# Optimization experiments

Measured on AMD Instinct MI355X. Metric: run time of the kernel, lower is better.

## Reference

```python
import jax, jax.numpy as jnp
import numpy as np

N_LOC = 500000
N_CAT = 5000
N_EDGES = 2000000
LOC_DIM = 128
CAT_DIM = 128
INITRANGE = 0.1
NEG_SLOPE = 0.2


def setup_inputs() -> dict:
    key = jax.random.key(0)
    k1, k2, k3, k4 = jax.random.split(key, 4)
    loc_emb = jax.random.normal(k1, (N_LOC, LOC_DIM), dtype=jnp.float32)
    # loc_to_cat Linear params, init per init_weights(): uniform(-0.1, 0.1) weight, zero bias
    W = jax.random.uniform(k2, (CAT_DIM, LOC_DIM), dtype=jnp.float32,
                           minval=-INITRANGE, maxval=INITRANGE)
    b = jnp.zeros((CAT_DIM,), dtype=jnp.float32)
    edge_src = jax.random.randint(k3, (N_EDGES,), 0, N_LOC, dtype=jnp.int64)
    edge_dst = jax.random.randint(k4, (N_EDGES,), 0, N_CAT, dtype=jnp.int64)
    return {"loc_emb": loc_emb, "W": W, "b": b,
            "edge_src": edge_src, "edge_dst": edge_dst}


def reference(loc_emb, W, b, edge_src, edge_dst):
    # copy_u('f','m') + sum('m','in') across all canonical etypes, combined with 'sum':
    # gather source (loc) features along edges, segment-sum into cat nodes.
    msg = loc_emb[edge_src]                                   # [E, loc_dim]
    agg = jax.ops.segment_sum(msg, edge_dst, num_segments=N_CAT)  # [n_cat, loc_dim]
    # loc_to_cat linear + LeakyReLU(0.2)
    cat_emb = jax.nn.leaky_relu(agg @ W.T + b, negative_slope=NEG_SLOPE)
    return cat_emb
```

## Files before the change

### kernel.cpp

```cpp
#include <hip/hip_runtime.h>

#define N_LOC   500000
#define N_CAT   5000
#define N_EDGES 2000000
#define DIM     128
#define NEG_SLOPE 0.2f
#define PAD     5008
#define NB      128
#define EPB     15628

__launch_bounds__(1024)
__global__ void blockhist_kernel(const int* __restrict__ edst, const float* __restrict__ W,
                                 float* __restrict__ WT, int* __restrict__ rank,
                                 int* __restrict__ bhist) {
    int b = blockIdx.x, t = threadIdx.x;
    if (b == NB) {
        for (int i = t; i < DIM * DIM; i += 1024) {
            int j = i >> 7, k = i & 127;
            WT[k * DIM + j] = W[j * DIM + k];
        }
        return;
    }
    __shared__ int lh[N_CAT];
    for (int c = t; c < N_CAT; c += 1024) lh[c] = 0;
    __syncthreads();
    int s = b * EPB;
    int e = min(s + EPB, N_EDGES);
    int i = s + 4 * t;
    for (; i + 4 <= e; i += 4096) {
        int4 d = *(const int4*)(edst + i);
        int4 r;
        r.x = atomicAdd(&lh[d.x], 1);
        r.y = atomicAdd(&lh[d.y], 1);
        r.z = atomicAdd(&lh[d.z], 1);
        r.w = atomicAdd(&lh[d.w], 1);
        *(int4*)(rank + i) = r;
    }
    if (i < e) {
        int lim = min(i + 4, e);
        for (int j = i; j < lim; ++j) rank[j] = atomicAdd(&lh[edst[j]], 1);
    }
    __syncthreads();
    for (int c = t; c < N_CAT; c += 1024)
        bhist[(size_t)b * N_CAT + c] = lh[c];
}

__launch_bounds__(256)
__global__ void blockscan_kernel(int* __restrict__ bhist, int* __restrict__ tot) {
    int c = blockIdx.x * 256 + threadIdx.x;
    if (c >= N_CAT) return;
    int run = 0;
    for (int b0 = 0; b0 < NB; b0 += 8) {
        int v0 = bhist[(size_t)(b0 + 0) * N_CAT + c];
        int v1 = bhist[(size_t)(b0 + 1) * N_CAT + c];
        int v2 = bhist[(size_t)(b0 + 2) * N_CAT + c];
        int v3 = bhist[(size_t)(b0 + 3) * N_CAT + c];
        int v4 = bhist[(size_t)(b0 + 4) * N_CAT + c];
        int v5 = bhist[(size_t)(b0 + 5) * N_CAT + c];
        int v6 = bhist[(size_t)(b0 + 6) * N_CAT + c];
        int v7 = bhist[(size_t)(b0 + 7) * N_CAT + c];
        bhist[(size_t)(b0 + 0) * N_CAT + c] = run; run += v0;
        bhist[(size_t)(b0 + 1) * N_CAT + c] = run; run += v1;
        bhist[(size_t)(b0 + 2) * N_CAT + c] = run; run += v2;
        bhist[(size_t)(b0 + 3) * N_CAT + c] = run; run += v3;
        bhist[(size_t)(b0 + 4) * N_CAT + c] = run; run += v4;
        bhist[(size_t)(b0 + 5) * N_CAT + c] = run; run += v5;
        bhist[(size_t)(b0 + 6) * N_CAT + c] = run; run += v6;
        bhist[(size_t)(b0 + 7) * N_CAT + c] = run; run += v7;
    }
    tot[c] = run;
}

__launch_bounds__(1024)
__global__ void scan_kernel(const int* __restrict__ cnt, int* __restrict__ offsets) {
    __shared__ int wsum[16];
    __shared__ int woff[16];
    __shared__ int total_s, running_s;
    int t = threadIdx.x;
    int lane = t & 63, w = t >> 6;
    if (t == 0) { running_s = 0; offsets[0] = 0; }
    __syncthreads();
    for (int base = 0; base < N_CAT; base += 1024) {
        int i = base + t;
        int v = (i < N_CAT) ? cnt[i] : 0;
        int incl = v;
        #pragma unroll
        for (int off = 1; off < 64; off <<= 1) {
            int x = __shfl_up(incl, off, 64);
            if (lane >= off) incl += x;
        }
        if (lane == 63) wsum[w] = incl;
        __syncthreads();
        if (w == 0 && lane < 16) {
            int s = wsum[lane];
            int e = s;
            #pragma unroll
            for (int off = 1; off < 16; off <<= 1) {
                int x = __shfl_up(e, off, 64);
                if (lane >= off) e += x;
            }
            woff[lane] = e - s;
            if (lane == 15) total_s = e;
        }
        __syncthreads();
        int run = running_s;
        if (i < N_CAT) offsets[i + 1] = run + woff[w] + incl;
        __syncthreads();
        if (t == 0) running_s = run + total_s;
        __syncthreads();
    }
}

__global__ void fill2_kernel(const int* __restrict__ esrc, const int* __restrict__ edst,
                             const int* __restrict__ rank, const int* __restrict__ offsets,
                             const int* __restrict__ bhist, int* __restrict__ csr_src) {
    int i4 = (blockIdx.x * blockDim.x + threadIdx.x) * 4;
    if (i4 + 4 <= N_EDGES) {
        int4 c = *(const int4*)(edst + i4);
        int4 s = *(const int4*)(esrc + i4);
        int4 r = *(const int4*)(rank + i4);
        size_t bb = (size_t)(i4 / EPB) * N_CAT;
        csr_src[offsets[c.x] + bhist[bb + c.x] + r.x] = s.x;
        csr_src[offsets[c.y] + bhist[bb + c.y] + r.y] = s.y;
        csr_src[offsets[c.z] + bhist[bb + c.z] + r.z] = s.z;
        csr_src[offsets[c.w] + bhist[bb + c.w] + r.w] = s.w;
    } else {
        for (int i = i4; i < N_EDGES; ++i) {
            int c = edst[i];
            size_t bb = (size_t)(i / EPB) * N_CAT;
            csr_src[offsets[c] + bhist[bb + c] + rank[i]] = esrc[i];
        }
    }
}

__launch_bounds__(256)
__global__ void agg_fused_kernel(const float* __restrict__ loc, const int* __restrict__ csr_src,
                                 const int* __restrict__ offsets, const float* __restrict__ WT,
                                 const float* __restrict__ bias, float* __restrict__ out) {
    __shared__ float4 sacc[256];
    __shared__ float  srow[DIM];
    int c = blockIdx.x;
    int t = threadIdx.x;
    int g = t >> 5;
    int l = t & 31;
    int beg = offsets[c];
    int end = offsets[c + 1];
    int cnt = end - beg;
    int per = (cnt + 7) >> 3;
    int gbeg = beg + g * per;
    int gend = min(gbeg + per, end);

    float4 a0 = make_float4(0.f, 0.f, 0.f, 0.f);
    float4 a1 = make_float4(0.f, 0.f, 0.f, 0.f);
    float4 a2 = make_float4(0.f, 0.f, 0.f, 0.f);
    float4 a3 = make_float4(0.f, 0.f, 0.f, 0.f);
    int e = gbeg;
    for (; e + 8 <= gend; e += 8) {
        int s0 = csr_src[e + 0], s1 = csr_src[e + 1], s2 = csr_src[e + 2], s3 = csr_src[e + 3];
        int s4 = csr_src[e + 4], s5 = csr_src[e + 5], s6 = csr_src[e + 6], s7 = csr_src[e + 7];
        float4 v0 = ((const float4*)(loc + (size_t)s0 * DIM))[l];
        float4 v1 = ((const float4*)(loc + (size_t)s1 * DIM))[l];
        float4 v2 = ((const float4*)(loc + (size_t)s2 * DIM))[l];
        float4 v3 = ((const float4*)(loc + (size_t)s3 * DIM))[l];
        float4 v4 = ((const float4*)(loc + (size_t)s4 * DIM))[l];
        float4 v5 = ((const float4*)(loc + (size_t)s5 * DIM))[l];
        float4 v6 = ((const float4*)(loc + (size_t)s6 * DIM))[l];
        float4 v7 = ((const float4*)(loc + (size_t)s7 * DIM))[l];
        a0.x += v0.x; a0.y += v0.y; a0.z += v0.z; a0.w += v0.w;
        a1.x += v1.x; a1.y += v1.y; a1.z += v1.z; a1.w += v1.w;
        a2.x += v2.x; a2.y += v2.y; a2.z += v2.z; a2.w += v2.w;
        a3.x += v3.x; a3.y += v3.y; a3.z += v3.z; a3.w += v3.w;
        a0.x += v4.x; a0.y += v4.y; a0.z += v4.z; a0.w += v4.w;
        a1.x += v5.x; a1.y += v5.y; a1.z += v5.z; a1.w += v5.w;
        a2.x += v6.x; a2.y += v6.y; a2.z += v6.z; a2.w += v6.w;
        a3.x += v7.x; a3.y += v7.y; a3.z += v7.z; a3.w += v7.w;
    }
    for (; e + 4 <= gend; e += 4) {
        int s0 = csr_src[e + 0], s1 = csr_src[e + 1], s2 = csr_src[e + 2], s3 = csr_src[e + 3];
        float4 v0 = ((const float4*)(loc + (size_t)s0 * DIM))[l];
        float4 v1 = ((const float4*)(loc + (size_t)s1 * DIM))[l];
        float4 v2 = ((const float4*)(loc + (size_t)s2 * DIM))[l];
        float4 v3 = ((const float4*)(loc + (size_t)s3 * DIM))[l];
        a0.x += v0.x; a0.y += v0.y; a0.z += v0.z; a0.w += v0.w;
        a1.x += v1.x; a1.y += v1.y; a1.z += v1.z; a1.w += v1.w;
        a2.x += v2.x; a2.y += v2.y; a2.z += v2.z; a2.w += v2.w;
        a3.x += v3.x; a3.y += v3.y; a3.z += v3.z; a3.w += v3.w;
    }
    for (; e < gend; ++e) {
        int s = csr_src[e];
        float4 v = ((const float4*)(loc + (size_t)s * DIM))[l];
        a0.x += v.x; a0.y += v.y; a0.z += v.z; a0.w += v.w;
    }
    float4 acc = make_float4((a0.x + a1.x) + (a2.x + a3.x),
                             (a0.y + a1.y) + (a2.y + a3.y),
                             (a0.z + a1.z) + (a2.z + a3.z),
                             (a0.w + a1.w) + (a2.w + a3.w));
    sacc[t] = acc;
    __syncthreads();
    if (t < 128) {
        float4 a = sacc[t], b = sacc[t + 128];
        sacc[t] = make_float4(a.x + b.x, a.y + b.y, a.z + b.z, a.w + b.w);
    }
    __syncthreads();
    if (t < 64) {
        float4 a = sacc[t], b = sacc[t + 64];
        sacc[t] = make_float4(a.x + b.x, a.y + b.y, a.z + b.z, a.w + b.w);
    }
    __syncthreads();
    if (t < 32) {
        float4 a = sacc[t], b = sacc[t + 32];
        srow[4 * t + 0] = a.x + b.x;
        srow[4 * t + 1] = a.y + b.y;
        srow[4 * t + 2] = a.z + b.z;
        srow[4 * t + 3] = a.w + b.w;
    }
    __syncthreads();
    int j = t & 127;
    int h = t >> 7;
    float m0 = 0.f, m1 = 0.f, m2 = 0.f, m3 = 0.f;
    int k0 = h * 64;
    #pragma unroll 4
    for (int k = 0; k < 64; k += 4) {
        m0 += WT[(k0 + k + 0) * DIM + j] * srow[k0 + k + 0];
        m1 += WT[(k0 + k + 1) * DIM + j] * srow[k0 + k + 1];
        m2 += WT[(k0 + k + 2) * DIM + j] * srow[k0 + k + 2];
        m3 += WT[(k0 + k + 3) * DIM + j] * srow[k0 + k + 3];
    }
    float* sred = (float*)sacc;
    sred[t] = (m0 + m1) + (m2 + m3);
    __syncthreads();
    if (t < 128) {
        float v = sred[t] + sred[t + 128] + bias[t];
        v = v > 0.f ? v : NEG_SLOPE * v;
        out[(size_t)c * DIM + t] = v;
    }
}


__global__ void hist_rank_kernel(const int* __restrict__ dst, int* __restrict__ cnt,
                                 int* __restrict__ rank, int n) {
    int i = blockIdx.x * blockDim.x + threadIdx.x;
    if (i < n) rank[i] = atomicAdd(&cnt[dst[i]], 1);
}

__global__ void fill_rank_kernel(const int* __restrict__ src, const int* __restrict__ dst,
                                 const int* __restrict__ rank, const int* __restrict__ offsets,
                                 int* __restrict__ csr_src, int n) {
    int i = blockIdx.x * blockDim.x + threadIdx.x;
    if (i < n) csr_src[offsets[dst[i]] + rank[i]] = src[i];
}

__global__ void transpose_kernel(const float* __restrict__ W, float* __restrict__ WT) {
    int j = blockIdx.x;
    int k = threadIdx.x;
    WT[k * DIM + j] = W[j * DIM + k];
}

__global__ void zero_kernel(float* p, int n) {
    int i = blockIdx.x * blockDim.x + threadIdx.x;
    if (i < n) p[i] = 0.f;
}

__launch_bounds__(128)
__global__ void scatter_atomic_kernel(const float* __restrict__ loc, const int* __restrict__ src,
                                      const int* __restrict__ dst, float* __restrict__ agg) {
    int e = blockIdx.x;
    int d = threadIdx.x;
    atomicAdd(&agg[(size_t)dst[e] * DIM + d], loc[(size_t)src[e] * DIM + d]);
}

#define CATS_PER_BLOCK 8
__launch_bounds__(256)
__global__ void gemm_lrelu_kernel(const float* __restrict__ agg, const float* __restrict__ W,
                                  const float* __restrict__ b, float* __restrict__ out) {
    __shared__ float sW[DIM * 129];
    __shared__ float sA[CATS_PER_BLOCK * DIM];
    int t = threadIdx.x;
    int cbase = blockIdx.x * CATS_PER_BLOCK;
    for (int i = t; i < DIM * DIM; i += 256) {
        int j = i >> 7, k = i & 127;
        sW[j * 129 + k] = W[i];
    }
    for (int i = t; i < CATS_PER_BLOCK * DIM; i += 256)
        sA[i] = agg[(size_t)cbase * DIM + i];
    __syncthreads();
    int j = t & 127;
    int cc = t >> 7;
    float acc0 = 0.f, acc1 = 0.f, acc2 = 0.f, acc3 = 0.f;
    for (int k = 0; k < DIM; ++k) {
        float w = sW[j * 129 + k];
        acc0 += w * sA[(cc + 0) * DIM + k];
        acc1 += w * sA[(cc + 2) * DIM + k];
        acc2 += w * sA[(cc + 4) * DIM + k];
        acc3 += w * sA[(cc + 6) * DIM + k];
    }
    float bj = b[j];
    float r0 = acc0 + bj, r1 = acc1 + bj, r2 = acc2 + bj, r3 = acc3 + bj;
    r0 = r0 > 0.f ? r0 : NEG_SLOPE * r0;
    r1 = r1 > 0.f ? r1 : NEG_SLOPE * r1;
    r2 = r2 > 0.f ? r2 : NEG_SLOPE * r2;
    r3 = r3 > 0.f ? r3 : NEG_SLOPE * r3;
    out[(size_t)(cbase + cc + 0) * DIM + j] = r0;
    out[(size_t)(cbase + cc + 2) * DIM + j] = r1;
    out[(size_t)(cbase + cc + 4) * DIM + j] = r2;
    out[(size_t)(cbase + cc + 6) * DIM + j] = r3;
}

extern "C" void kernel_launch(void* const* d_in, const int* in_sizes, int n_in,
                              void* d_out, int out_size, void* d_ws, size_t ws_size,
                              hipStream_t stream) {
    const float* loc  = (const float*)d_in[0];
    const float* W    = (const float*)d_in[1];
    const float* bias = (const float*)d_in[2];
    const int*   esrc = (const int*)d_in[3];
    const int*   edst = (const int*)d_in[4];
    float* out = (float*)d_out;

    size_t need_cs   = ((size_t)2 * N_EDGES + (size_t)NB * N_CAT + 3 * PAD + DIM * DIM) * sizeof(int);
    size_t need_rank = ((size_t)2 * N_EDGES + 2 * PAD + DIM * DIM) * sizeof(int);

    if (ws_size >= need_cs) {
        int*   rank    = (int*)d_ws;
        int*   csr_src = rank + N_EDGES;
        int*   bhist   = csr_src + N_EDGES;
        int*   tot     = bhist + (size_t)NB * N_CAT;
        int*   offsets = tot + PAD;
        float* WT      = (float*)(offsets + PAD);

        blockhist_kernel<<<NB + 1, 1024, 0, stream>>>(edst, W, WT, rank, bhist);
        blockscan_kernel<<<(N_CAT + 255) / 256, 256, 0, stream>>>(bhist, tot);
        scan_kernel<<<1, 1024, 0, stream>>>(tot, offsets);
        fill2_kernel<<<(N_EDGES / 4 + 255) / 256, 256, 0, stream>>>(esrc, edst, rank, offsets, bhist, csr_src);
        agg_fused_kernel<<<N_CAT, 256, 0, stream>>>(loc, csr_src, offsets, WT, bias, out);
    } else if (ws_size >= need_rank) {
        int* counts  = (int*)d_ws;
        int* offsets = counts + PAD;
        float* WT    = (float*)(offsets + PAD);
        int* rank    = (int*)(WT + DIM * DIM);
        int* csr_src = rank + N_EDGES;

        hipMemsetAsync(counts, 0, (size_t)PAD * sizeof(int), stream);
        transpose_kernel<<<DIM, DIM, 0, stream>>>(W, WT);
        const int eblocks = (N_EDGES + 255) / 256;
        hist_rank_kernel<<<eblocks, 256, 0, stream>>>(edst, counts, rank, N_EDGES);
        scan_kernel<<<1, 1024, 0, stream>>>(counts, offsets);
        fill_rank_kernel<<<eblocks, 256, 0, stream>>>(esrc, edst, rank, offsets, csr_src, N_EDGES);
        agg_fused_kernel<<<N_CAT, 256, 0, stream>>>(loc, csr_src, offsets, WT, bias, out);
    } else {
        int n = N_CAT * DIM;
        zero_kernel<<<(n + 255) / 256, 256, 0, stream>>>(out, n);
        scatter_atomic_kernel<<<N_EDGES, DIM, 0, stream>>>(loc, esrc, edst, out);
        gemm_lrelu_kernel<<<N_CAT / CATS_PER_BLOCK, 256, 0, stream>>>(out, W, bias, out);
    }
}
```

Measured before the change: 493.9 us.

## Replace global CSR build with per-block local sort and segmented aggregation

The old histogram, block-scan, global-scan and scatter-fill pipeline becomes a single build kernel. Each of the 128 edge chunks is counting-sorted by destination in shared memory and written out with per-chunk offsets. The aggregation kernel then walks each destination's 16 chunk segments per warp group instead of one contiguous global CSR range. This cuts three launches, the rank array traffic and the random global scatter, and the aggregation blocks are remapped to interleave categories. In exchange the aggregation does more small, irregular segment loops with extra offset loads. The 8-way unrolled loop in the fallback kernel is also removed.

```diff
diff --git a/kernel.cpp b/kernel.cpp
--- a/kernel.cpp
+++ b/kernel.cpp
@@ -8,11 +8,12 @@
 #define PAD     5008
 #define NB      128
 #define EPB     15628
+#define NC1     (N_CAT + 1)
 
 __launch_bounds__(1024)
-__global__ void blockhist_kernel(const int* __restrict__ edst, const float* __restrict__ W,
-                                 float* __restrict__ WT, int* __restrict__ rank,
-                                 int* __restrict__ bhist) {
+__global__ void build_kernel(const int* __restrict__ esrc, const int* __restrict__ edst,
+                             const float* __restrict__ W, float* __restrict__ WT,
+                             int* __restrict__ csr2, int* __restrict__ loffg) {
     int b = blockIdx.x, t = threadIdx.x;
     if (b == NB) {
         for (int i = t; i < DIM * DIM; i += 1024) {
@@ -22,53 +23,191 @@
         return;
     }
     __shared__ int lh[N_CAT];
-    for (int c = t; c < N_CAT; c += 1024) lh[c] = 0;
-    __syncthreads();
-    int s = b * EPB;
-    int e = min(s + EPB, N_EDGES);
-    int i = s + 4 * t;
-    for (; i + 4 <= e; i += 4096) {
-        int4 d = *(const int4*)(edst + i);
-        int4 r;
-        r.x = atomicAdd(&lh[d.x], 1);
-        r.y = atomicAdd(&lh[d.y], 1);
-        r.z = atomicAdd(&lh[d.z], 1);
-        r.w = atomicAdd(&lh[d.w], 1);
-        *(int4*)(rank + i) = r;
-    }
-    if (i < e) {
-        int lim = min(i + 4, e);
-        for (int j = i; j < lim; ++j) rank[j] = atomicAdd(&lh[edst[j]], 1);
-    }
-    __syncthreads();
-    for (int c = t; c < N_CAT; c += 1024)
-        bhist[(size_t)b * N_CAT + c] = lh[c];
+    __shared__ __align__(16) int sbuf[EPB];
+    __shared__ int wsum[16], woff[16];
+
+    for (int c2 = t; c2 < N_CAT; c2 += 1024) lh[c2] = 0;
+    __syncthreads();
+
+    const int s0 = b * EPB;
+    const int len = min(s0 + EPB, N_EDGES) - s0;
+    const int* dp = edst + s0;
+    const int* sp = esrc + s0;
+
+    #pragma unroll
+    for (int j = 0; j < 4; ++j) {
+        int off = j * 4096 + 4 * t;
+        if (off < len) {
+            int4 d = *(const int4*)(dp + off);
+            atomicAdd(&lh[d.x], 1); atomicAdd(&lh[d.y], 1);
+            atomicAdd(&lh[d.z], 1); atomicAdd(&lh[d.w], 1);
+        }
+    }
+    __syncthreads();
+
+    int lane = t & 63, w = t >> 6;
+    int base = t * 5;
+    int v0 = 0, v1 = 0, v2 = 0, v3 = 0, v4 = 0;
+    if (base < N_CAT) { v0 = lh[base]; v1 = lh[base+1]; v2 = lh[base+2]; v3 = lh[base+3]; v4 = lh[base+4]; }
+    int sum = v0 + v1 + v2 + v3 + v4;
+    int incl = sum;
+    #pragma unroll
+    for (int o = 1; o < 64; o <<= 1) { int x = __shfl_up(incl, o, 64); if (lane >= o) incl += x; }
+    if (lane == 63) wsum[w] = incl;
+    __syncthreads();
+    if (t < 16) {
+        int sv = wsum[t]; int ev = sv;
+        #pragma unroll
+        for (int o = 1; o < 16; o <<= 1) { int x = __shfl_up(ev, o, 64); if (t >= o) ev += x; }
+        woff[t] = ev - sv;
+    }
+    __syncthreads();
+    if (base < N_CAT) {
+        int run = woff[w] + (incl - sum);
+        lh[base]     = run; run += v0;
+        lh[base + 1] = run; run += v1;
+        lh[base + 2] = run; run += v2;
+        lh[base + 3] = run; run += v3;
+        lh[base + 4] = run;
+    }
+    __syncthreads();
+
+    for (int c2 = t; c2 < N_CAT; c2 += 1024) loffg[(size_t)b * NC1 + c2] = lh[c2];
+    if (t == 0) loffg[(size_t)b * NC1 + N_CAT] = len;
+    __syncthreads();
+
+    #pragma unroll
+    for (int j = 0; j < 4; ++j) {
+        int off = j * 4096 + 4 * t;
+        if (off < len) {
+            int4 d = *(const int4*)(dp + off);
+            int4 s = *(const int4*)(sp + off);
+            int p0 = atomicAdd(&lh[d.x], 1); sbuf[p0] = s.x;
+            int p1 = atomicAdd(&lh[d.y], 1); sbuf[p1] = s.y;
+            int p2 = atomicAdd(&lh[d.z], 1); sbuf[p2] = s.z;
+            int p3 = atomicAdd(&lh[d.w], 1); sbuf[p3] = s.w;
+        }
+    }
+    __syncthreads();
+
+    int* cout = csr2 + s0;
+    for (int i = 4 * t; i < len; i += 4096)
+        *(int4*)(cout + i) = *(const int4*)(sbuf + i);
 }
 
 __launch_bounds__(256)
-__global__ void blockscan_kernel(int* __restrict__ bhist, int* __restrict__ tot) {
-    int c = blockIdx.x * 256 + threadIdx.x;
-    if (c >= N_CAT) return;
-    int run = 0;
-    for (int b0 = 0; b0 < NB; b0 += 8) {
-        int v0 = bhist[(size_t)(b0 + 0) * N_CAT + c];
-        int v1 = bhist[(size_t)(b0 + 1) * N_CAT + c];
-        int v2 = bhist[(size_t)(b0 + 2) * N_CAT + c];
-        int v3 = bhist[(size_t)(b0 + 3) * N_CAT + c];
-        int v4 = bhist[(size_t)(b0 + 4) * N_CAT + c];
-        int v5 = bhist[(size_t)(b0 + 5) * N_CAT + c];
-        int v6 = bhist[(size_t)(b0 + 6) * N_CAT + c];
-        int v7 = bhist[(size_t)(b0 + 7) * N_CAT + c];
-        bhist[(size_t)(b0 + 0) * N_CAT + c] = run; run += v0;
-        bhist[(size_t)(b0 + 1) * N_CAT + c] = run; run += v1;
-        bhist[(size_t)(b0 + 2) * N_CAT + c] = run; run += v2;
-        bhist[(size_t)(b0 + 3) * N_CAT + c] = run; run += v3;
-        bhist[(size_t)(b0 + 4) * N_CAT + c] = run; run += v4;
-        bhist[(size_t)(b0 + 5) * N_CAT + c] = run; run += v5;
-        bhist[(size_t)(b0 + 6) * N_CAT + c] = run; run += v6;
-        bhist[(size_t)(b0 + 7) * N_CAT + c] = run; run += v7;
-    }
-    tot[c] = run;
+__global__ void agg2_kernel(const float* __restrict__ loc, const int* __restrict__ csr2,
+                            const int* __restrict__ loffg, const float* __restrict__ WT,
+                            const float* __restrict__ bias, float* __restrict__ out) {
+    __shared__ float4 sacc[256];
+    __shared__ float  srow[DIM];
+    int bid = blockIdx.x;
+    int c = (bid & 7) * (N_CAT / 8) + (bid >> 3);
+    int t = threadIdx.x;
+    int g = t >> 5;
+    int l = t & 31;
+
+    float4 a0 = make_float4(0.f, 0.f, 0.f, 0.f);
+    float4 a1 = a0, a2 = a0, a3 = a0;
+
+    int bb = g * (NB / 8);
+    int s = loffg[(size_t)bb * NC1 + c];
+    int e = loffg[(size_t)bb * NC1 + c + 1];
+    for (int ib = 0; ib < NB / 8; ++ib) {
+        int ns = 0, ne = 0;
+        if (ib + 1 < NB / 8) {
+            ns = loffg[(size_t)(bb + 1) * NC1 + c];
+            ne = loffg[(size_t)(bb + 1) * NC1 + c + 1];
+        }
+        const int* cp = csr2 + (size_t)bb * EPB;
+        int p = s;
+        for (; p + 4 <= e; p += 4) {
+            int s0 = cp[p], s1 = cp[p + 1], s2 = cp[p + 2], s3 = cp[p + 3];
+            float4 v0 = ((const float4*)(loc + (size_t)s0 * DIM))[l];
+            float4 v1 = ((const float4*)(loc + (size_t)s1 * DIM))[l];
+            float4 v2 = ((const float4*)(loc + (size_t)s2 * DIM))[l];
+            float4 v3 = ((const float4*)(loc + (size_t)s3 * DIM))[l];
+            a0.x += v0.x; a0.y += v0.y; a0.z += v0.z; a0.w += v0.w;
+            a1.x += v1.x; a1.y += v1.y; a1.z += v1.z; a1.w += v1.w;
+            a2.x += v2.x; a2.y += v2.y; a2.z += v2.z; a2.w += v2.w;
+            a3.x += v3.x; a3.y += v3.y; a3.z += v3.z; a3.w += v3.w;
+        }
+        for (; p < e; ++p) {
+            int sx = cp[p];
+            float4 v = ((const float4*)(loc + (size_t)sx * DIM))[l];
+            a0.x += v.x; a0.y += v.y; a0.z += v.z; a0.w += v.w;
+        }
+        s = ns; e = ne; ++bb;
+    }
+
+    float4 acc = make_float4((a0.x + a1.x) + (a2.x + a3.x),
+                             (a0.y + a1.y) + (a2.y + a3.y),
+                             (a0.z + a1.z) + (a2.z + a3.z),
+                             (a0.w + a1.w) + (a2.w + a3.w));
+    sacc[t] = acc;
+    __syncthreads();
+    if (t < 128) {
+        float4 a = sacc[t], b = sacc[t + 128];
+        sacc[t] = make_float4(a.x + b.x, a.y + b.y, a.z + b.z, a.w + b.w);
+    }
+    __syncthreads();
+    if (t < 64) {
+        float4 a = sacc[t], b = sacc[t + 64];
+        sacc[t] = make_float4(a.x + b.x, a.y + b.y, a.z + b.z, a.w + b.w);
+    }
+    __syncthreads();
+    if (t < 32) {
+        float4 a = sacc[t], b = sacc[t + 32];
+        srow[4 * t + 0] = a.x + b.x;
+        srow[4 * t + 1] = a.y + b.y;
+        srow[4 * t + 2] = a.z + b.z;
+        srow[4 * t + 3] = a.w + b.w;
+    }
+    __syncthreads();
+    int j = t & 127;
+    int h = t >> 7;
+    float m0 = 0.f, m1 = 0.f, m2 = 0.f, m3 = 0.f;
+    int k0 = h * 64;
+    #pragma unroll 4
+    for (int k = 0; k < 64; k += 4) {
+        m0 += WT[(k0 + k + 0) * DIM + j] * srow[k0 + k + 0];
+        m1 += WT[(k0 + k + 1) * DIM + j] * srow[k0 + k + 1];
+        m2 += WT[(k0 + k + 2) * DIM + j] * srow[k0 + k + 2];
+        m3 += WT[(k0 + k + 3) * DIM + j] * srow[k0 + k + 3];
+    }
+    float* sred = (float*)sacc;
+    sred[t] = (m0 + m1) + (m2 + m3);
+    __syncthreads();
+    if (t < 128) {
+        float v = sred[t] + sred[t + 128] + bias[t];
+        v = v > 0.f ? v : NEG_SLOPE * v;
+        out[(size_t)c * DIM + t] = v;
+    }
+}
+
+
+__global__ void hist_rank_kernel(const int* __restrict__ dst, int* __restrict__ cnt,
+                                 int* __restrict__ rank, int n) {
+    int i = blockIdx.x * blockDim.x + threadIdx.x;
+    if (i < n) rank[i] = atomicAdd(&cnt[dst[i]], 1);
+}
+
+__global__ void fill_rank_kernel(const int* __restrict__ src, const int* __restrict__ dst,
+                                 const int* __restrict__ rank, const int* __restrict__ offsets,
+                                 int* __restrict__ csr_src, int n) {
+    int i = blockIdx.x * blockDim.x + threadIdx.x;
+    if (i < n) csr_src[offsets[dst[i]] + rank[i]] = src[i];
+}
+
+__global__ void transpose_kernel(const float* __restrict__ W, float* __restrict__ WT) {
+    int j = blockIdx.x;
+    int k = threadIdx.x;
+    WT[k * DIM + j] = W[j * DIM + k];
+}
+
+__global__ void zero_kernel(float* p, int n) {
+    int i = blockIdx.x * blockDim.x + threadIdx.x;
+    if (i < n) p[i] = 0.f;
 }
 
 __launch_bounds__(1024)
@@ -108,28 +247,6 @@
         __syncthreads();
         if (t == 0) running_s = run + total_s;
         __syncthreads();
-    }
-}
-
-__global__ void fill2_kernel(const int* __restrict__ esrc, const int* __restrict__ edst,
-                             const int* __restrict__ rank, const int* __restrict__ offsets,
-                             const int* __restrict__ bhist, int* __restrict__ csr_src) {
-    int i4 = (blockIdx.x * blockDim.x + threadIdx.x) * 4;
-    if (i4 + 4 <= N_EDGES) {
-        int4 c = *(const int4*)(edst + i4);
-        int4 s = *(const int4*)(esrc + i4);
-        int4 r = *(const int4*)(rank + i4);
-        size_t bb = (size_t)(i4 / EPB) * N_CAT;
-        csr_src[offsets[c.x] + bhist[bb + c.x] + r.x] = s.x;
-        csr_src[offsets[c.y] + bhist[bb + c.y] + r.y] = s.y;
-        csr_src[offsets[c.z] + bhist[bb + c.z] + r.z] = s.z;
-        csr_src[offsets[c.w] + bhist[bb + c.w] + r.w] = s.w;
-    } else {
-        for (int i = i4; i < N_EDGES; ++i) {
-            int c = edst[i];
-            size_t bb = (size_t)(i / EPB) * N_CAT;
-            csr_src[offsets[c] + bhist[bb + c] + rank[i]] = esrc[i];
-        }
     }
 }
 
@@ -151,30 +268,8 @@
     int gend = min(gbeg + per, end);
 
     float4 a0 = make_float4(0.f, 0.f, 0.f, 0.f);
-    float4 a1 = make_float4(0.f, 0.f, 0.f, 0.f);
-    float4 a2 = make_float4(0.f, 0.f, 0.f, 0.f);
-    float4 a3 = make_float4(0.f, 0.f, 0.f, 0.f);
+    float4 a1 = a0, a2 = a0, a3 = a0;
     int e = gbeg;
-    for (; e + 8 <= gend; e += 8) {
-        int s0 = csr_src[e + 0], s1 = csr_src[e + 1], s2 = csr_src[e + 2], s3 = csr_src[e + 3];
-        int s4 = csr_src[e + 4], s5 = csr_src[e + 5], s6 = csr_src[e + 6], s7 = csr_src[e + 7];
-        float4 v0 = ((const float4*)(loc + (size_t)s0 * DIM))[l];
-        float4 v1 = ((const float4*)(loc + (size_t)s1 * DIM))[l];
-        float4 v2 = ((const float4*)(loc + (size_t)s2 * DIM))[l];
-        float4 v3 = ((const float4*)(loc + (size_t)s3 * DIM))[l];
-        float4 v4 = ((const float4*)(loc + (size_t)s4 * DIM))[l];
-        float4 v5 = ((const float4*)(loc + (size_t)s5 * DIM))[l];
-        float4 v6 = ((const float4*)(loc + (size_t)s6 * DIM))[l];
-        float4 v7 = ((const float4*)(loc + (size_t)s7 * DIM))[l];
-        a0.x += v0.x; a0.y += v0.y; a0.z += v0.z; a0.w += v0.w;
-        a1.x += v1.x; a1.y += v1.y; a1.z += v1.z; a1.w += v1.w;
-        a2.x += v2.x; a2.y += v2.y; a2.z += v2.z; a2.w += v2.w;
-        a3.x += v3.x; a3.y += v3.y; a3.z += v3.z; a3.w += v3.w;
-        a0.x += v4.x; a0.y += v4.y; a0.z += v4.z; a0.w += v4.w;
-        a1.x += v5.x; a1.y += v5.y; a1.z += v5.z; a1.w += v5.w;
-        a2.x += v6.x; a2.y += v6.y; a2.z += v6.z; a2.w += v6.w;
-        a3.x += v7.x; a3.y += v7.y; a3.z += v7.z; a3.w += v7.w;
-    }
     for (; e + 4 <= gend; e += 4) {
         int s0 = csr_src[e + 0], s1 = csr_src[e + 1], s2 = csr_src[e + 2], s3 = csr_src[e + 3];
         float4 v0 = ((const float4*)(loc + (size_t)s0 * DIM))[l];
@@ -234,31 +329,6 @@
         v = v > 0.f ? v : NEG_SLOPE * v;
         out[(size_t)c * DIM + t] = v;
     }
-}
-
-
-__global__ void hist_rank_kernel(const int* __restrict__ dst, int* __restrict__ cnt,
-                                 int* __restrict__ rank, int n) {
-    int i = blockIdx.x * blockDim.x + threadIdx.x;
-    if (i < n) rank[i] = atomicAdd(&cnt[dst[i]], 1);
-}
-
-__global__ void fill_rank_kernel(const int* __restrict__ src, const int* __restrict__ dst,
-                                 const int* __restrict__ rank, const int* __restrict__ offsets,
-                                 int* __restrict__ csr_src, int n) {
-    int i = blockIdx.x * blockDim.x + threadIdx.x;
-    if (i < n) csr_src[offsets[dst[i]] + rank[i]] = src[i];
-}
-
-__global__ void transpose_kernel(const float* __restrict__ W, float* __restrict__ WT) {
-    int j = blockIdx.x;
-    int k = threadIdx.x;
-    WT[k * DIM + j] = W[j * DIM + k];
-}
-
-__global__ void zero_kernel(float* p, int n) {
-    int i = blockIdx.x * blockDim.x + threadIdx.x;
-    if (i < n) p[i] = 0.f;
 }
 
 __launch_bounds__(128)
@@ -316,22 +386,16 @@
     const int*   edst = (const int*)d_in[4];
     float* out = (float*)d_out;
 
-    size_t need_cs   = ((size_t)2 * N_EDGES + (size_t)NB * N_CAT + 3 * PAD + DIM * DIM) * sizeof(int);
+    size_t need_new  = ((size_t)N_EDGES + (size_t)NB * NC1 + DIM * DIM) * sizeof(int);
     size_t need_rank = ((size_t)2 * N_EDGES + 2 * PAD + DIM * DIM) * sizeof(int);
 
-    if (ws_size >= need_cs) {
-        int*   rank    = (int*)d_ws;
-        int*   csr_src = rank + N_EDGES;
-        int*   bhist   = csr_src + N_EDGES;
-        int*   tot     = bhist + (size_t)NB * N_CAT;
-        int*   offsets = tot + PAD;
-        float* WT      = (float*)(offsets + PAD);
-
-        blockhist_kernel<<<NB + 1, 1024, 0, stream>>>(edst, W, WT, rank, bhist);
-        blockscan_kernel<<<(N_CAT + 255) / 256, 256, 0, stream>>>(bhist, tot);
-        scan_kernel<<<1, 1024, 0, stream>>>(tot, offsets);
-        fill2_kernel<<<(N_EDGES / 4 + 255) / 256, 256, 0, stream>>>(esrc, edst, rank, offsets, bhist, csr_src);
-        agg_fused_kernel<<<N_CAT, 256, 0, stream>>>(loc, csr_src, offsets, WT, bias, out);
+    if (ws_size >= need_new) {
+        int*   csr2  = (int*)d_ws;
+        int*   loffg = csr2 + N_EDGES;
+        float* WT    = (float*)(loffg + (size_t)NB * NC1);
+
+        build_kernel<<<NB + 1, 1024, 0, stream>>>(esrc, edst, W, WT, csr2, loffg);
+        agg2_kernel<<<N_CAT, 256, 0, stream>>>(loc, csr2, loffg, WT, bias, out);
     } else if (ws_size >= need_rank) {
         int* counts  = (int*)d_ws;
         int* offsets = counts + PAD;
```

Measured after the change: 473.8 us. 1.04x faster.
